# Kernel tuning notes

Measured on AMD Instinct MI355X. Metric: run time of the kernel, lower is better.

## Reference

```python
import jax, jax.numpy as jnp
import numpy as np

BLOCK_SIZE = 256

def setup_inputs() -> dict:
    key = jax.random.key(0)
    k1, k2, k3, k4 = jax.random.split(key, 4)
    B, T, C, H = 128, 256, 1024, 128
    x = jax.random.normal(k1, (B, T, C), dtype=jnp.float32)
    Wk = jax.random.normal(k2, (C, H), dtype=jnp.float32) * 0.02
    Wq = jax.random.normal(k3, (C, H), dtype=jnp.float32) * 0.02
    Wv = jax.random.normal(k4, (C, H), dtype=jnp.float32) * 0.02
    return {"x": x, "Wk": Wk, "Wq": Wq, "Wv": Wv}

def reference(x, Wk, Wq, Wv):
    B, T, C = x.shape
    k = x @ Wk  # [B,T,H]
    q = x @ Wq  # [B,T,H]
    v = x @ Wv  # [B,T,H]
    # NOTE: source scales by C**-0.5 (input channels), not head_size**-0.5
    scale = jnp.asarray(C, x.dtype) ** -0.5
    wei = jnp.einsum('bth,bsh->bts', q, k) * scale  # [B,T,T]
    causal = jnp.tril(jnp.ones((T, T), dtype=bool))
    wei = jnp.where(causal, wei, -jnp.inf)
    wei = jax.nn.softmax(wei, axis=-1)
    # keras Dropout is identity in inference mode
    out = jnp.einsum('bts,bsh->bth', wei, v)  # [B,T,H]
    return out
```

## Files before the change

### kernel.cpp

```cpp
#include <hip/hip_runtime.h>
#include <hip/hip_bf16.h>
#include <stdint.h>


typedef __attribute__((ext_vector_type(4))) float    floatx4;
typedef __attribute__((ext_vector_type(4))) float    float4v;
typedef __attribute__((ext_vector_type(8))) short    short8;
typedef __attribute__((ext_vector_type(4))) short    short4v;
typedef __attribute__((ext_vector_type(2))) unsigned uint2v;

__device__ __forceinline__ short f2bf(float f) {
  unsigned u = __builtin_bit_cast(unsigned, f);
  unsigned r = (u + 0x7FFFu + ((u >> 16) & 1u)) >> 16;
  return (short)(unsigned short)r;
}

__device__ __forceinline__ unsigned cvt2(float a, float b) {
  __hip_bfloat162 h = __float22bfloat162_rn(make_float2(a, b));
  unsigned u;
  __builtin_memcpy(&u, &h, 4);
  return u;
}

#if defined(__has_builtin)
#if __has_builtin(__builtin_amdgcn_global_load_lds)
#define HAVE_GLDS 1
#endif
#endif

__global__ void wconv_kernel(const float* __restrict__ Wk, const float* __restrict__ Wq,
                             const float* __restrict__ Wv, short* __restrict__ Wt) {
  int n = blockIdx.x;
  const float* W = (n < 128) ? Wq : ((n < 256) ? Wk : Wv);
  int col = n & 127;
  int base = n << 10;
  for (int c = threadIdx.x; c < 1024; c += blockDim.x)
    Wt[base + c] = f2bf(W[(c << 7) + col]);
}

__global__ __launch_bounds__(256, 3) void proj_kernel(
    const float* __restrict__ x, const short* __restrict__ Wt,
    short* __restrict__ qb, short* __restrict__ kb, short* __restrict__ vT) {
  __shared__ short As[128 * 64];
  __shared__ short Bs[128 * 64];
  const int tid  = threadIdx.x;
  const int lane = tid & 63;
  const int wv   = tid >> 6;
  const int wm   = wv >> 1;
  const int wn   = wv & 1;
  const int Lb   = ((blockIdx.x & 7) * 96) + (blockIdx.x >> 3);
  const int mblk = Lb / 3;
  const int nblk = Lb - mblk * 3;
  const int m0   = mblk << 7;
  const int n0   = nblk << 7;

  const int l15 = lane & 15;
  const int kg  = lane >> 4;
  const int rr  = lane >> 3;
  const int swB = ((lane & 7) ^ rr) << 3;

  const floatx4 fz = {0.f, 0.f, 0.f, 0.f};
  floatx4 acc[4][4];
#pragma unroll
  for (int a = 0; a < 4; ++a)
#pragma unroll
    for (int bb = 0; bb < 4; ++bb) acc[a][bb] = fz;

  float4v xr[8];

#define LOAD_A(K0)                                                                    \
  _Pragma("unroll") for (int it = 0; it < 8; ++it) {                                  \
    int idx = (it << 8) + tid;                                                        \
    int row = idx >> 4, c4 = idx & 15;                                                \
    xr[it] = *reinterpret_cast<const float4v*>(x + (size_t)(m0 + row) * 1024 +        \
                                               (K0) + (c4 << 2));                     \
  }

#define CVT_WRITE_A()                                                                 \
  _Pragma("unroll") for (int it = 0; it < 8; ++it) {                                  \
    int idx = (it << 8) + tid;                                                        \
    int row = idx >> 4, c4 = idx & 15;                                                \
    uint2v u;                                                                         \
    u[0] = cvt2(xr[it][0], xr[it][1]);                                                \
    u[1] = cvt2(xr[it][2], xr[it][3]);                                                \
    int pb = (row << 7) + (((c4 << 3)) ^ ((row & 7) << 4));                           \
    *reinterpret_cast<uint2v*>(reinterpret_cast<char*>(As) + pb) = u;                 \
  }

#ifdef HAVE_GLDS
#define STAGE_B(K0)                                                                   \
  _Pragma("unroll") for (int i = 0; i < 4; ++i) {                                     \
    int row0 = (wv << 5) + (i << 3);                                                  \
    __builtin_amdgcn_global_load_lds(                                                 \
        (const __attribute__((address_space(1))) unsigned int*)(const void*)(         \
            Wt + ((size_t)(n0 + row0 + rr) << 10) + (K0) + swB),                      \
        (__attribute__((address_space(3))) unsigned int*)(void*)(&Bs[row0 << 6]),     \
        16, 0, 0);                                                                    \
  }
#else
#define STAGE_B(K0)                                                                   \
  _Pragma("unroll") for (int i = 0; i < 4; ++i) {                                     \
    int row = (wv << 5) + (i << 3) + rr;                                              \
    short8 w8 = *reinterpret_cast<const short8*>(Wt + ((size_t)(n0 + row) << 10) +    \
                                                 (K0) + ((lane & 7) << 3));           \
    int pb = (row << 7) + ((((lane & 7) << 4)) ^ ((row & 7) << 4));                   \
    *reinterpret_cast<short8*>(reinterpret_cast<char*>(Bs) + pb) = w8;                \
  }
#endif

  LOAD_A(0)

#pragma unroll 1
  for (int kt = 0; kt < 16; ++kt) {
    const int k0 = kt << 6;
    __syncthreads();
    STAGE_B(k0)
    CVT_WRITE_A()
    if (kt < 15) LOAD_A(k0 + 64)
    __syncthreads();
#pragma unroll
    for (int ks = 0; ks < 2; ++ks) {
      short8 af[4], bfr[4];
#pragma unroll
      for (int mf = 0; mf < 4; ++mf) {
        int row = (wm << 6) + (mf << 4) + l15;
        int pb = (row << 7) + ((((ks << 6) + (kg << 4))) ^ ((row & 7) << 4));
        af[mf] = *reinterpret_cast<const short8*>(reinterpret_cast<const char*>(As) + pb);
      }
#pragma unroll
      for (int nf = 0; nf < 4; ++nf) {
        int n = (wn << 6) + (nf << 4) + l15;
        int pb = (n << 7) + ((((ks << 6) + (kg << 4))) ^ ((n & 7) << 4));
        bfr[nf] = *reinterpret_cast<const short8*>(reinterpret_cast<const char*>(Bs) + pb);
      }
#pragma unroll
      for (int mf = 0; mf < 4; ++mf)
#pragma unroll
        for (int nf = 0; nf < 4; ++nf)
          acc[mf][nf] =
              __builtin_amdgcn_mfma_f32_16x16x32_bf16(af[mf], bfr[nf], acc[mf][nf], 0, 0, 0);
    }
  }

#pragma unroll
  for (int mf = 0; mf < 4; ++mf) {
#pragma unroll
    for (int nf = 0; nf < 4; ++nf) {
#pragma unroll
      for (int r = 0; r < 4; ++r) {
        int m  = m0 + (wm << 6) + (mf << 4) + (kg << 2) + r;
        int ng = n0 + (wn << 6) + (nf << 4) + l15;
        short bv = f2bf(acc[mf][nf][r]);
        int h = ng & 127;
        if (ng < 128)      qb[(size_t)m * 128 + h] = bv;
        else if (ng < 256) kb[(size_t)m * 128 + h] = bv;
        else               vT[((size_t)(m >> 8) << 15) + (h << 8) + (m & 255)] = bv;
      }
    }
  }
#undef LOAD_A
#undef CVT_WRITE_A
#undef STAGE_B
}

__global__ __launch_bounds__(64, 2) void attn_kernel(
    const short* __restrict__ q, const short* __restrict__ k,
    const short* __restrict__ vT, float* __restrict__ out) {
  __shared__ short P[16 * 64];
  const int lane = threadIdx.x;
  const int b    = blockIdx.x >> 4;
  const int w    = blockIdx.x & 15;
  const int qr0  = w << 4;
  const short* qb = q  + ((size_t)b << 15);
  const short* kb = k  + ((size_t)b << 15);
  const short* vb = vT + ((size_t)b << 15);

  short8 qf[4];
  {
    int row = qr0 + (lane & 15);
#pragma unroll
    for (int hs = 0; hs < 4; ++hs)
      qf[hs] = *reinterpret_cast<const short8*>(qb + row * 128 + (hs << 5) + ((lane >> 4) << 3));
  }
  const floatx4 fz = {0.f, 0.f, 0.f, 0.f};
  floatx4 o[8];
#pragma unroll
  for (int i = 0; i < 8; ++i) o[i] = fz;
  float ls[4] = {0.f, 0.f, 0.f, 0.f};

  const int nt = ((w << 4) + 79) >> 6;
  for (int tt = 0; tt < nt; ++tt) {
    const int j0 = tt << 6;
    floatx4 s[4];
#pragma unroll
    for (int i = 0; i < 4; ++i) s[i] = fz;
#pragma unroll
    for (int nf = 0; nf < 4; ++nf) {
      int kr = j0 + (nf << 4) + (lane & 15);
#pragma unroll
      for (int hs = 0; hs < 4; ++hs) {
        short8 kf =
            *reinterpret_cast<const short8*>(kb + kr * 128 + (hs << 5) + ((lane >> 4) << 3));
        s[nf] = __builtin_amdgcn_mfma_f32_16x16x32_bf16(qf[hs], kf, s[nf], 0, 0, 0);
      }
    }
    const int ib = qr0 + ((lane >> 4) << 2);
#pragma unroll
    for (int nf = 0; nf < 4; ++nf) {
      int j = j0 + (nf << 4) + (lane & 15);
#pragma unroll
      for (int r = 0; r < 4; ++r) {
        float p = (j <= ib + r) ? __expf(s[nf][r] * 0.03125f) : 0.f;
        ls[r] += p;
        int prow = ((lane >> 4) << 2) + r;
        int pb = (prow << 7) + (((((nf << 4) + (lane & 15)) << 1)) ^ ((prow & 7) << 4));
        *reinterpret_cast<short*>(reinterpret_cast<char*>(P) + pb) = f2bf(p);
      }
    }
    __syncthreads();
    short8 pa[2];
#pragma unroll
    for (int ks = 0; ks < 2; ++ks) {
      int prow = lane & 15;
      int pb = (prow << 7) + ((((ks << 6) + ((lane >> 4) << 4))) ^ ((prow & 7) << 4));
      pa[ks] = *reinterpret_cast<const short8*>(reinterpret_cast<const char*>(P) + pb);
    }
#pragma unroll
    for (int hf = 0; hf < 8; ++hf) {
#pragma unroll
      for (int ks = 0; ks < 2; ++ks) {
        int vrow = (hf << 4) + (lane & 15);
        short8 vf = *reinterpret_cast<const short8*>(vb + (vrow << 8) + j0 + (ks << 5) +
                                                     ((lane >> 4) << 3));
        o[hf] = __builtin_amdgcn_mfma_f32_16x16x32_bf16(pa[ks], vf, o[hf], 0, 0, 0);
      }
    }
    __syncthreads();
  }
#pragma unroll
  for (int r = 0; r < 4; ++r) {
#pragma unroll
    for (int mk = 1; mk < 16; mk <<= 1) ls[r] += __shfl_xor(ls[r], mk);
  }
#pragma unroll
  for (int r = 0; r < 4; ++r) {
    float inv = 1.0f / ls[r];
    int t = qr0 + ((lane >> 4) << 2) + r;
#pragma unroll
    for (int hf = 0; hf < 8; ++hf)
      out[(((size_t)b << 8) + t) * 128 + (hf << 4) + (lane & 15)] = o[hf][r] * inv;
  }
}

extern "C" void kernel_launch(void* const* d_in, const int* in_sizes, int n_in,
                              void* d_out, int out_size, void* d_ws, size_t ws_size,
                              hipStream_t stream) {
  const float* x  = (const float*)d_in[0];
  const float* Wk = (const float*)d_in[1];
  const float* Wq = (const float*)d_in[2];
  const float* Wv = (const float*)d_in[3];
  float* out = (float*)d_out;

  char* ws = (char*)d_ws;
  short* Wt = (short*)ws;
  short* qb = (short*)(ws + 786432);
  short* kb = (short*)(ws + 786432 + 8388608);
  short* vT = (short*)(ws + 786432 + 2 * 8388608);

  wconv_kernel<<<384, 256, 0, stream>>>(Wk, Wq, Wv, Wt);
  proj_kernel<<<768, 256, 0, stream>>>(x, Wt, qb, kb, vT);
  attn_kernel<<<128 * 16, 64, 0, stream>>>(qb, kb, vT, out);
}
```

Baseline: 95.71 us.

## Compute all QKV columns per block with double-buffered pipelined projection

Each projection block now covers a 128-row tile across all 384 q/k/v output columns with 8 waves, so the fp32 input is loaded and converted to bf16 once instead of three times. The K loop is double-buffered in LDS with hand-placed vmcnt/lgkmcnt waits, raw barriers and MFMA priority raising, overlapping next-tile global loads with current MFMAs. The larger LDS footprint and a grid of 256 blocks reduce occupancy, and the manual wait counts add correctness risk.

Measured after the change: 95.35 us. Within noise of the previous version (-0.4%).

```diff
diff --git a/kernel.cpp b/kernel.cpp
--- a/kernel.cpp
+++ b/kernel.cpp
@@ -27,6 +27,10 @@
 #define HAVE_GLDS 1
 #endif
 #endif
+
+#define SBAR()  __builtin_amdgcn_s_barrier()
+#define LGKM0() do { asm volatile("s_waitcnt lgkmcnt(0)" ::: "memory"); \
+                     __builtin_amdgcn_sched_barrier(0); } while (0)
 
 __global__ void wconv_kernel(const float* __restrict__ Wk, const float* __restrict__ Wq,
                              const float* __restrict__ Wv, short* __restrict__ Wt) {
@@ -38,21 +42,17 @@
     Wt[base + c] = f2bf(W[(c << 7) + col]);
 }
 
-__global__ __launch_bounds__(256, 3) void proj_kernel(
+__global__ __launch_bounds__(512, 2) void proj_kernel(
     const float* __restrict__ x, const short* __restrict__ Wt,
     short* __restrict__ qb, short* __restrict__ kb, short* __restrict__ vT) {
-  __shared__ short As[128 * 64];
-  __shared__ short Bs[128 * 64];
+  __shared__ short As[2][128 * 64];
+  __shared__ short Bs[2][384 * 64];
   const int tid  = threadIdx.x;
   const int lane = tid & 63;
   const int wv   = tid >> 6;
-  const int wm   = wv >> 1;
-  const int wn   = wv & 1;
-  const int Lb   = ((blockIdx.x & 7) * 96) + (blockIdx.x >> 3);
-  const int mblk = Lb / 3;
-  const int nblk = Lb - mblk * 3;
-  const int m0   = mblk << 7;
-  const int n0   = nblk << 7;
+  const int wm   = wv >> 2;
+  const int wn   = wv & 3;
+  const int m0   = blockIdx.x << 7;
 
   const int l15 = lane & 15;
   const int kg  = lane >> 4;
@@ -60,96 +60,127 @@
   const int swB = ((lane & 7) ^ rr) << 3;
 
   const floatx4 fz = {0.f, 0.f, 0.f, 0.f};
-  floatx4 acc[4][4];
+  floatx4 acc[4][6];
 #pragma unroll
   for (int a = 0; a < 4; ++a)
 #pragma unroll
-    for (int bb = 0; bb < 4; ++bb) acc[a][bb] = fz;
-
-  float4v xr[8];
+    for (int bb = 0; bb < 6; ++bb) acc[a][bb] = fz;
+
+  float4v xr[4];
 
 #define LOAD_A(K0)                                                                    \
-  _Pragma("unroll") for (int it = 0; it < 8; ++it) {                                  \
-    int idx = (it << 8) + tid;                                                        \
+  _Pragma("unroll") for (int it = 0; it < 4; ++it) {                                  \
+    int idx = (it << 9) + tid;                                                        \
     int row = idx >> 4, c4 = idx & 15;                                                \
     xr[it] = *reinterpret_cast<const float4v*>(x + (size_t)(m0 + row) * 1024 +        \
                                                (K0) + (c4 << 2));                     \
   }
 
-#define CVT_WRITE_A()                                                                 \
-  _Pragma("unroll") for (int it = 0; it < 8; ++it) {                                  \
-    int idx = (it << 8) + tid;                                                        \
+#define CVT_WRITE_A(dst)                                                              \
+  _Pragma("unroll") for (int it = 0; it < 4; ++it) {                                  \
+    int idx = (it << 9) + tid;                                                        \
     int row = idx >> 4, c4 = idx & 15;                                                \
     uint2v u;                                                                         \
     u[0] = cvt2(xr[it][0], xr[it][1]);                                                \
     u[1] = cvt2(xr[it][2], xr[it][3]);                                                \
     int pb = (row << 7) + (((c4 << 3)) ^ ((row & 7) << 4));                           \
-    *reinterpret_cast<uint2v*>(reinterpret_cast<char*>(As) + pb) = u;                 \
+    *reinterpret_cast<uint2v*>(reinterpret_cast<char*>(dst) + pb) = u;                \
   }
 
 #ifdef HAVE_GLDS
-#define STAGE_B(K0)                                                                   \
-  _Pragma("unroll") for (int i = 0; i < 4; ++i) {                                     \
-    int row0 = (wv << 5) + (i << 3);                                                  \
+#define STAGE_B(dst, K0)                                                              \
+  _Pragma("unroll") for (int i = 0; i < 6; ++i) {                                     \
+    int row0 = wv * 48 + (i << 3);                                                    \
     __builtin_amdgcn_global_load_lds(                                                 \
         (const __attribute__((address_space(1))) unsigned int*)(const void*)(         \
-            Wt + ((size_t)(n0 + row0 + rr) << 10) + (K0) + swB),                      \
-        (__attribute__((address_space(3))) unsigned int*)(void*)(&Bs[row0 << 6]),     \
+            Wt + ((size_t)(row0 + rr) << 10) + (K0) + swB),                           \
+        (__attribute__((address_space(3))) unsigned int*)(void*)((dst) + (row0 << 6)),\
         16, 0, 0);                                                                    \
   }
 #else
-#define STAGE_B(K0)                                                                   \
-  _Pragma("unroll") for (int i = 0; i < 4; ++i) {                                     \
-    int row = (wv << 5) + (i << 3) + rr;                                              \
-    short8 w8 = *reinterpret_cast<const short8*>(Wt + ((size_t)(n0 + row) << 10) +    \
-                                                 (K0) + ((lane & 7) << 3));           \
+#define STAGE_B(dst, K0)                                                              \
+  _Pragma("unroll") for (int i = 0; i < 6; ++i) {                                     \
+    int row = wv * 48 + (i << 3) + rr;                                                \
+    short8 w8 = *reinterpret_cast<const short8*>(Wt + ((size_t)row << 10) + (K0) +    \
+                                                 ((lane & 7) << 3));                  \
     int pb = (row << 7) + ((((lane & 7) << 4)) ^ ((row & 7) << 4));                   \
-    *reinterpret_cast<short8*>(reinterpret_cast<char*>(Bs) + pb) = w8;                \
+    *reinterpret_cast<short8*>(reinterpret_cast<char*>(dst) + pb) = w8;               \
   }
 #endif
 
+#define READ_FRAGS(abuf, bbuf, KS)                                                    \
+  _Pragma("unroll") for (int mf = 0; mf < 4; ++mf) {                                  \
+    int row = (wm << 6) + (mf << 4) + l15;                                            \
+    int pb = (row << 7) + (((((KS) << 6) + (kg << 4))) ^ ((row & 7) << 4));           \
+    af[mf] = *reinterpret_cast<const short8*>(                                        \
+        reinterpret_cast<const char*>(abuf) + pb);                                    \
+  }                                                                                   \
+  _Pragma("unroll") for (int nf = 0; nf < 6; ++nf) {                                  \
+    int n = wn * 96 + (nf << 4) + l15;                                                \
+    int pb = (n << 7) + (((((KS) << 6) + (kg << 4))) ^ ((n & 7) << 4));               \
+    bfr[nf] = *reinterpret_cast<const short8*>(                                       \
+        reinterpret_cast<const char*>(bbuf) + pb);                                    \
+  }
+
+#define MFMA24()                                                                      \
+  _Pragma("unroll") for (int mf = 0; mf < 4; ++mf)                                    \
+  _Pragma("unroll") for (int nf = 0; nf < 6; ++nf)                                    \
+    acc[mf][nf] = __builtin_amdgcn_mfma_f32_16x16x32_bf16(af[mf], bfr[nf],            \
+                                                          acc[mf][nf], 0, 0, 0);
+
   LOAD_A(0)
+  STAGE_B(&Bs[0][0], 0)
+  asm volatile("s_waitcnt vmcnt(6)" ::: "memory");
+  __builtin_amdgcn_sched_barrier(0);
+  CVT_WRITE_A(&As[0][0])
+  LGKM0();
+  SBAR();
 
 #pragma unroll 1
   for (int kt = 0; kt < 16; ++kt) {
-    const int k0 = kt << 6;
-    __syncthreads();
-    STAGE_B(k0)
-    CVT_WRITE_A()
-    if (kt < 15) LOAD_A(k0 + 64)
-    __syncthreads();
-#pragma unroll
-    for (int ks = 0; ks < 2; ++ks) {
-      short8 af[4], bfr[4];
-#pragma unroll
-      for (int mf = 0; mf < 4; ++mf) {
-        int row = (wm << 6) + (mf << 4) + l15;
-        int pb = (row << 7) + ((((ks << 6) + (kg << 4))) ^ ((row & 7) << 4));
-        af[mf] = *reinterpret_cast<const short8*>(reinterpret_cast<const char*>(As) + pb);
-      }
-#pragma unroll
-      for (int nf = 0; nf < 4; ++nf) {
-        int n = (wn << 6) + (nf << 4) + l15;
-        int pb = (n << 7) + ((((ks << 6) + (kg << 4))) ^ ((n & 7) << 4));
-        bfr[nf] = *reinterpret_cast<const short8*>(reinterpret_cast<const char*>(Bs) + pb);
-      }
-#pragma unroll
-      for (int mf = 0; mf < 4; ++mf)
-#pragma unroll
-        for (int nf = 0; nf < 4; ++nf)
-          acc[mf][nf] =
-              __builtin_amdgcn_mfma_f32_16x16x32_bf16(af[mf], bfr[nf], acc[mf][nf], 0, 0, 0);
-    }
+    const int cur = kt & 1;
+    const int nxt = cur ^ 1;
+    const short* Ac = &As[cur][0];
+    const short* Bc = &Bs[cur][0];
+    short8 af[4], bfr[6];
+
+    if (kt < 15) {
+      LOAD_A((kt + 1) << 6)
+      asm volatile("s_waitcnt vmcnt(4)" ::: "memory");
+    } else {
+      asm volatile("s_waitcnt vmcnt(0)" ::: "memory");
+    }
+    __builtin_amdgcn_sched_barrier(0);
+    READ_FRAGS(Ac, Bc, 0)
+    if (kt < 15) STAGE_B(&Bs[nxt][0], (kt + 1) << 6)
+    SBAR();
+    LGKM0();
+    __builtin_amdgcn_s_setprio(1);
+    MFMA24()
+    __builtin_amdgcn_s_setprio(0);
+    SBAR();
+
+    READ_FRAGS(Ac, Bc, 1)
+    if (kt < 15) {
+      asm volatile("s_waitcnt vmcnt(6)" ::: "memory");
+      __builtin_amdgcn_sched_barrier(0);
+      CVT_WRITE_A(&As[nxt][0])
+    }
+    LGKM0();
+    __builtin_amdgcn_s_setprio(1);
+    MFMA24()
+    __builtin_amdgcn_s_setprio(0);
+    SBAR();
   }
 
 #pragma unroll
   for (int mf = 0; mf < 4; ++mf) {
 #pragma unroll
-    for (int nf = 0; nf < 4; ++nf) {
+    for (int nf = 0; nf < 6; ++nf) {
 #pragma unroll
       for (int r = 0; r < 4; ++r) {
         int m  = m0 + (wm << 6) + (mf << 4) + (kg << 2) + r;
-        int ng = n0 + (wn << 6) + (nf << 4) + l15;
+        int ng = wn * 96 + (nf << 4) + l15;
         short bv = f2bf(acc[mf][nf][r]);
         int h = ng & 127;
         if (ng < 128)      qb[(size_t)m * 128 + h] = bv;
@@ -161,6 +192,8 @@
 #undef LOAD_A
 #undef CVT_WRITE_A
 #undef STAGE_B
+#undef READ_FRAGS
+#undef MFMA24
 }
 
 __global__ __launch_bounds__(64, 2) void attn_kernel(
@@ -268,6 +301,6 @@
   short* vT = (short*)(ws + 786432 + 2 * 8388608);
 
   wconv_kernel<<<384, 256, 0, stream>>>(Wk, Wq, Wv, Wt);
-  proj_kernel<<<768, 256, 0, stream>>>(x, Wt, qb, kb, vT);
+  proj_kernel<<<256, 512, 0, stream>>>(x, Wt, qb, kb, vT);
   attn_kernel<<<128 * 16, 64, 0, stream>>>(qb, kb, vT, out);
 }
```
